# Kernel tuning notes

Measured on AMD Instinct MI355X. Metric: run time of the kernel, lower is better.

Reference implementation:

```python
import jax, jax.numpy as jnp
import numpy as np
import math

S = 30.0
M = 0.5
COS_M = math.cos(M)
SIN_M = math.sin(M)
TH = math.cos(math.pi - M)  # threshold cos(pi - m)
EPS = 1e-12  # matches F.normalize default eps


def setup_inputs() -> dict:
    key = jax.random.key(0)
    k1, k2, k3 = jax.random.split(key, 3)
    B, D, C = 1024, 512, 100000
    inp = jax.random.normal(k1, (B, D), dtype=jnp.float32)
    label = jax.random.randint(k2, (B,), 0, C)
    # xavier_uniform_ for weight of shape (C, D): bound = sqrt(6/(C+D))
    bound = math.sqrt(6.0 / (C + D))
    weight = jax.random.uniform(k3, (C, D), dtype=jnp.float32, minval=-bound, maxval=bound)
    return {"input": inp, "label": label, "weight": weight}


def _l2norm(x):
    # F.normalize: x / max(||x||, eps)
    n = jnp.sqrt(jnp.sum(x * x, axis=-1, keepdims=True))
    return x / jnp.maximum(n, EPS)


def reference(input, label, weight):
    # cosine: [B, C]
    cosine = jnp.einsum('bd,cd->bc', _l2norm(input), _l2norm(weight))
    sine = jnp.sqrt(jnp.clip(1.0 - cosine * cosine, 0.0, 1.0))
    phi = cosine * COS_M - sine * SIN_M
    phi = jnp.where(cosine > TH, phi, cosine - S * SIN_M * M)
    # one-hot combine done via direct label-indexed select (avoids materializing one_hot)
    B, C = cosine.shape
    is_target = jnp.arange(C)[None, :] == label[:, None]  # [B, C] bool
    output = jnp.where(is_target, phi, cosine) * S
    return output
```

## Files before the change

### kernel.cpp

```cpp
#include <hip/hip_runtime.h>
#include <hip/hip_bf16.h>


#define MDIM 1024
#define KDIM 512
#define NCLS 100000

#define BM 128
#define BN 128
#define BK 32
#define LDST 40

typedef unsigned short u16;
typedef unsigned int u32;
typedef short s16x8 __attribute__((ext_vector_type(8)));
typedef float f32x4 __attribute__((ext_vector_type(4)));

__device__ __forceinline__ u32 pk2(float a, float b) {
  u32 ua = __builtin_bit_cast(u32, a);
  u32 ub = __builtin_bit_cast(u32, b);
  ua += 0x7FFFu + ((ua >> 16) & 1u);
  ub += 0x7FFFu + ((ub >> 16) & 1u);
  return (ua >> 16) | (ub & 0xFFFF0000u);
}

__global__ __launch_bounds__(256) void norm_input_kernel(const float* __restrict__ in,
                                                         u16* __restrict__ abf) {
  const int row = blockIdx.x;
  const int tid = threadIdx.x;
  const float2 v = *reinterpret_cast<const float2*>(in + (size_t)row * KDIM + 2 * tid);
  float ss = v.x * v.x + v.y * v.y;
#pragma unroll
  for (int off = 32; off > 0; off >>= 1) ss += __shfl_down(ss, off);
  __shared__ float part[4];
  if ((tid & 63) == 0) part[tid >> 6] = ss;
  __syncthreads();
  const float tot = part[0] + part[1] + part[2] + part[3];
  const float rn = 1.0f / fmaxf(sqrtf(tot), 1e-12f);
  reinterpret_cast<u32*>(abf)[row * (KDIM / 2) + tid] = pk2(v.x * rn, v.y * rn);
}

__global__ __launch_bounds__(256) void arcface_gemm(const u16* __restrict__ Abf,
                                                    const float* __restrict__ W,
                                                    const int* __restrict__ label,
                                                    float* __restrict__ out) {
  __shared__ u16 lA[BM * LDST];
  __shared__ u16 lW[BN * LDST];
  __shared__ float rnw[BN];
  __shared__ int lbl[BM];

  const int tid = threadIdx.x;
  const int m0 = blockIdx.x * BM;
  const int n0 = blockIdx.y * BN;

  if (tid < BM) lbl[tid] = label[m0 + tid];

  const int r = tid >> 1;
  const int half = tid & 1;
  int c = n0 + r;
  if (c >= NCLS) c = NCLS - 1;

  const u16* aptr = Abf + (size_t)(m0 + r) * KDIM + half * 16;
  const float* wptr = W + (size_t)c * KDIM + half * 16;

  uint4 a0 = *(const uint4*)(aptr);
  uint4 a1 = *(const uint4*)(aptr + 8);
  float4 w0 = *(const float4*)(wptr);
  float4 w1 = *(const float4*)(wptr + 4);
  float4 w2 = *(const float4*)(wptr + 8);
  float4 w3 = *(const float4*)(wptr + 12);

  f32x4 acc[4][4] = {};
  float ss = 0.0f;

  const int lane = tid & 63;
  const int wv = tid >> 6;
  const int wm = (wv & 1) * 64;
  const int wn = (wv >> 1) * 64;
  const int ln = lane & 15;
  const int kq = lane >> 4;

  const int aw = r * LDST + half * 16;

  for (int kt = 0; kt < KDIM / BK; ++kt) {
    __syncthreads();
    *(uint4*)&lA[aw] = a0;
    *(uint4*)&lA[aw + 8] = a1;
    ss += w0.x * w0.x + w0.y * w0.y + w0.z * w0.z + w0.w * w0.w;
    ss += w1.x * w1.x + w1.y * w1.y + w1.z * w1.z + w1.w * w1.w;
    ss += w2.x * w2.x + w2.y * w2.y + w2.z * w2.z + w2.w * w2.w;
    ss += w3.x * w3.x + w3.y * w3.y + w3.z * w3.z + w3.w * w3.w;
    uint4 p0, p1;
    p0.x = pk2(w0.x, w0.y); p0.y = pk2(w0.z, w0.w);
    p0.z = pk2(w1.x, w1.y); p0.w = pk2(w1.z, w1.w);
    p1.x = pk2(w2.x, w2.y); p1.y = pk2(w2.z, w2.w);
    p1.z = pk2(w3.x, w3.y); p1.w = pk2(w3.z, w3.w);
    *(uint4*)&lW[aw] = p0;
    *(uint4*)&lW[aw + 8] = p1;
    __syncthreads();

    if (kt < KDIM / BK - 1) {
      const u16* ap = aptr + (kt + 1) * BK;
      a0 = *(const uint4*)(ap);
      a1 = *(const uint4*)(ap + 8);
      const float* wp = wptr + (kt + 1) * BK;
      w0 = *(const float4*)(wp);
      w1 = *(const float4*)(wp + 4);
      w2 = *(const float4*)(wp + 8);
      w3 = *(const float4*)(wp + 12);
    }

    s16x8 af[4], wf[4];
#pragma unroll
    for (int i = 0; i < 4; ++i)
      af[i] = *(const s16x8*)&lA[(wm + 16 * i + ln) * LDST + kq * 8];
#pragma unroll
    for (int j = 0; j < 4; ++j)
      wf[j] = *(const s16x8*)&lW[(wn + 16 * j + ln) * LDST + kq * 8];
#pragma unroll
    for (int i = 0; i < 4; ++i)
#pragma unroll
      for (int j = 0; j < 4; ++j)
        acc[i][j] = __builtin_amdgcn_mfma_f32_16x16x32_bf16(af[i], wf[j], acc[i][j], 0, 0, 0);
  }

  const float sst = ss + __shfl_xor(ss, 1);
  if (half == 0) rnw[r] = 1.0f / fmaxf(sqrtf(sst), 1e-12f);
  __syncthreads();

  constexpr float S_ = 30.0f;
  constexpr float COS_M = 0.87758256189037276f;
  constexpr float SIN_M = 0.47942553860420301f;
  constexpr float TH_ = -0.87758256189037276f;
  constexpr float FALLB = 30.0f * 0.47942553860420301f * 0.5f;

#pragma unroll
  for (int i = 0; i < 4; ++i) {
    const int lrow_b = wm + 16 * i + 4 * kq;
#pragma unroll
    for (int j = 0; j < 4; ++j) {
      const int col = wn + 16 * j + ln;
      const int gcol = n0 + col;
      const float rw = rnw[col];
      if (gcol < NCLS) {
#pragma unroll
        for (int rg = 0; rg < 4; ++rg) {
          const int lrow = lrow_b + rg;
          const float cosv = acc[i][j][rg] * rw;
          float o = S_ * cosv;
          if (gcol == lbl[lrow]) {
            const float s2 = fmaxf(1.0f - cosv * cosv, 0.0f);
            const float sine = sqrtf(s2);
            float phi = cosv * COS_M - sine * SIN_M;
            phi = (cosv > TH_) ? phi : (cosv - FALLB);
            o = S_ * phi;
          }
          out[(size_t)(m0 + lrow) * NCLS + gcol] = o;
        }
      }
    }
  }
}

extern "C" void kernel_launch(void* const* d_in, const int* in_sizes, int n_in,
                              void* d_out, int out_size, void* d_ws, size_t ws_size,
                              hipStream_t stream) {
  const float* input = (const float*)d_in[0];
  const int* label = (const int*)d_in[1];
  const float* weight = (const float*)d_in[2];
  float* out = (float*)d_out;
  u16* abf = (u16*)d_ws;

  hipLaunchKernelGGL(norm_input_kernel, dim3(MDIM), dim3(256), 0, stream, input, abf);
  dim3 grid(MDIM / BM, (NCLS + BN - 1) / BN);
  hipLaunchKernelGGL(arcface_gemm, grid, dim3(256), 0, stream, abf, weight, label, out);
}
```

Measured before the change: 767.6 us.

## Pre-normalize weights to bf16 and remap GEMM tiles for L2 reuse

Adds a separate kernel that normalizes each weight row and writes it as bf16 into workspace. The GEMM then loads bf16 weights directly, with no per-tile fp32 conversion or norm reduction. It also uses a 1D grid with a swizzled tile order, so the 8 M-tiles that share a weight tile run close together, and it writes the output with nontemporal stores. The cost is an extra pass that reads 200MB of fp32 weights and writes 100MB of bf16, and it needs enough workspace; otherwise the old path runs.

```diff
diff --git a/kernel.cpp b/kernel.cpp
--- a/kernel.cpp
+++ b/kernel.cpp
@@ -1,5 +1,4 @@
 #include <hip/hip_runtime.h>
-#include <hip/hip_bf16.h>
 
 
 #define MDIM 1024
@@ -10,6 +9,9 @@
 #define BN 128
 #define BK 32
 #define LDST 40
+
+#define NTILES ((NCLS + BN - 1) / BN)
+#define NWG (8 * NTILES)
 
 typedef unsigned short u16;
 typedef unsigned int u32;
@@ -38,6 +40,130 @@
   const float tot = part[0] + part[1] + part[2] + part[3];
   const float rn = 1.0f / fmaxf(sqrtf(tot), 1e-12f);
   reinterpret_cast<u32*>(abf)[row * (KDIM / 2) + tid] = pk2(v.x * rn, v.y * rn);
+}
+
+__global__ __launch_bounds__(256) void norm_weight_kernel(const float* __restrict__ W,
+                                                          u16* __restrict__ wbf) {
+  const int row = blockIdx.x * 4 + (threadIdx.x >> 6);
+  const int lane = threadIdx.x & 63;
+  const float* p = W + (size_t)row * KDIM + lane * 8;
+  const float4 v0 = *reinterpret_cast<const float4*>(p);
+  const float4 v1 = *reinterpret_cast<const float4*>(p + 4);
+  float ss = v0.x * v0.x + v0.y * v0.y + v0.z * v0.z + v0.w * v0.w
+           + v1.x * v1.x + v1.y * v1.y + v1.z * v1.z + v1.w * v1.w;
+#pragma unroll
+  for (int off = 32; off > 0; off >>= 1) ss += __shfl_xor(ss, off);
+  const float rn = 1.0f / fmaxf(sqrtf(ss), 1e-12f);
+  uint4 o;
+  o.x = pk2(v0.x * rn, v0.y * rn);
+  o.y = pk2(v0.z * rn, v0.w * rn);
+  o.z = pk2(v1.x * rn, v1.y * rn);
+  o.w = pk2(v1.z * rn, v1.w * rn);
+  *reinterpret_cast<uint4*>(wbf + (size_t)row * KDIM + lane * 8) = o;
+}
+
+__global__ __launch_bounds__(256) void arcface_gemm_bf16(const u16* __restrict__ Abf,
+                                                         const u16* __restrict__ Wbf,
+                                                         const int* __restrict__ label,
+                                                         float* __restrict__ out) {
+  __shared__ u16 lA[BM * LDST];
+  __shared__ u16 lW[BN * LDST];
+  __shared__ int lbl[BM];
+
+  const int tid = threadIdx.x;
+  const int orig = blockIdx.x;
+  const int wg = (orig & 7) * NTILES + (orig >> 3);
+  const int m0 = (wg & 7) * BM;
+  const int n0 = (wg >> 3) * BN;
+
+  if (tid < BM) lbl[tid] = label[m0 + tid];
+
+  const int r = tid >> 1;
+  const int half = tid & 1;
+  int c = n0 + r;
+  if (c >= NCLS) c = NCLS - 1;
+
+  const u16* aptr = Abf + (size_t)(m0 + r) * KDIM + half * 16;
+  const u16* wptr = Wbf + (size_t)c * KDIM + half * 16;
+
+  uint4 a0 = *(const uint4*)(aptr);
+  uint4 a1 = *(const uint4*)(aptr + 8);
+  uint4 b0 = *(const uint4*)(wptr);
+  uint4 b1 = *(const uint4*)(wptr + 8);
+
+  f32x4 acc[4][4] = {};
+
+  const int lane = tid & 63;
+  const int wv = tid >> 6;
+  const int wm = (wv & 1) * 64;
+  const int wn = (wv >> 1) * 64;
+  const int ln = lane & 15;
+  const int kq = lane >> 4;
+
+  const int aw = r * LDST + half * 16;
+
+  for (int kt = 0; kt < KDIM / BK; ++kt) {
+    __syncthreads();
+    *(uint4*)&lA[aw] = a0;
+    *(uint4*)&lA[aw + 8] = a1;
+    *(uint4*)&lW[aw] = b0;
+    *(uint4*)&lW[aw + 8] = b1;
+    __syncthreads();
+
+    if (kt < KDIM / BK - 1) {
+      const u16* ap = aptr + (kt + 1) * BK;
+      a0 = *(const uint4*)(ap);
+      a1 = *(const uint4*)(ap + 8);
+      const u16* wp = wptr + (kt + 1) * BK;
+      b0 = *(const uint4*)(wp);
+      b1 = *(const uint4*)(wp + 8);
+    }
+
+    s16x8 af[4], wf[4];
+#pragma unroll
+    for (int i = 0; i < 4; ++i)
+      af[i] = *(const s16x8*)&lA[(wm + 16 * i + ln) * LDST + kq * 8];
+#pragma unroll
+    for (int j = 0; j < 4; ++j)
+      wf[j] = *(const s16x8*)&lW[(wn + 16 * j + ln) * LDST + kq * 8];
+#pragma unroll
+    for (int i = 0; i < 4; ++i)
+#pragma unroll
+      for (int j = 0; j < 4; ++j)
+        acc[i][j] = __builtin_amdgcn_mfma_f32_16x16x32_bf16(af[i], wf[j], acc[i][j], 0, 0, 0);
+  }
+
+  constexpr float S_ = 30.0f;
+  constexpr float COS_M = 0.87758256189037276f;
+  constexpr float SIN_M = 0.47942553860420301f;
+  constexpr float TH_ = -0.87758256189037276f;
+  constexpr float FALLB = 30.0f * 0.47942553860420301f * 0.5f;
+
+#pragma unroll
+  for (int i = 0; i < 4; ++i) {
+    const int lrow_b = wm + 16 * i + 4 * kq;
+#pragma unroll
+    for (int j = 0; j < 4; ++j) {
+      const int col = wn + 16 * j + ln;
+      const int gcol = n0 + col;
+      if (gcol < NCLS) {
+#pragma unroll
+        for (int rg = 0; rg < 4; ++rg) {
+          const int lrow = lrow_b + rg;
+          const float cosv = acc[i][j][rg];
+          float o = S_ * cosv;
+          if (gcol == lbl[lrow]) {
+            const float s2 = fmaxf(1.0f - cosv * cosv, 0.0f);
+            const float sine = sqrtf(s2);
+            float phi = cosv * COS_M - sine * SIN_M;
+            phi = (cosv > TH_) ? phi : (cosv - FALLB);
+            o = S_ * phi;
+          }
+          __builtin_nontemporal_store(o, &out[(size_t)(m0 + lrow) * NCLS + gcol]);
+        }
+      }
+    }
+  }
 }
 
 __global__ __launch_bounds__(256) void arcface_gemm(const u16* __restrict__ Abf,
@@ -172,6 +298,15 @@
   u16* abf = (u16*)d_ws;
 
   hipLaunchKernelGGL(norm_input_kernel, dim3(MDIM), dim3(256), 0, stream, input, abf);
-  dim3 grid(MDIM / BM, (NCLS + BN - 1) / BN);
-  hipLaunchKernelGGL(arcface_gemm, grid, dim3(256), 0, stream, abf, weight, label, out);
-}
+
+  const size_t a_bytes = (size_t)MDIM * KDIM * sizeof(u16);
+  const size_t w_bytes = (size_t)NCLS * KDIM * sizeof(u16);
+  if (ws_size >= a_bytes + w_bytes) {
+    u16* wbf = abf + (size_t)MDIM * KDIM;
+    hipLaunchKernelGGL(norm_weight_kernel, dim3(NCLS / 4), dim3(256), 0, stream, weight, wbf);
+    hipLaunchKernelGGL(arcface_gemm_bf16, dim3(NWG), dim3(256), 0, stream, abf, wbf, label, out);
+  } else {
+    dim3 grid(MDIM / BM, (NCLS + BN - 1) / BN);
+    hipLaunchKernelGGL(arcface_gemm, grid, dim3(256), 0, stream, abf, weight, label, out);
+  }
+}
```

Measured after the change: 719.2 us. -6.3%, faster.
